# Optimization experiments

Hardware: AMD Instinct MI355X
Metric: run time of the kernel (lower is better)

The kernel has to match this reference:

```python
import jax, jax.numpy as jnp
import numpy as np

B, T, D, H = 4, 2048, 1024, 16
HD = D // H  # 64
EPS = 1e-5


def setup_inputs() -> dict:
    key = jax.random.key(0)
    ks = jax.random.split(key, 8)
    s = 0.02
    return {
        "X": jax.random.normal(ks[0], (B, T, D), dtype=jnp.float32),
        # per-head projection weights stacked: [H, D, HD] (no bias, matches nn.Linear(bias=False))
        "Wq": jax.random.normal(ks[1], (H, D, HD), dtype=jnp.float32) * s,
        "Wk": jax.random.normal(ks[2], (H, D, HD), dtype=jnp.float32) * s,
        "Wv": jax.random.normal(ks[3], (H, D, HD), dtype=jnp.float32) * s,
        "ln1_g": jnp.ones((D,), jnp.float32),
        "ln1_b": jnp.zeros((D,), jnp.float32),
        "W1": jax.random.normal(ks[4], (D, 4 * D), dtype=jnp.float32) * s,
        "b1": jnp.zeros((4 * D,), jnp.float32),
        "W2": jax.random.normal(ks[5], (4 * D, D), dtype=jnp.float32) * s,
        "b2": jnp.zeros((D,), jnp.float32),
        "ln2_g": jnp.ones((D,), jnp.float32),
        "ln2_b": jnp.zeros((D,), jnp.float32),
    }


def _layer_norm(x, g, b):
    m = jnp.mean(x, axis=-1, keepdims=True)
    v = jnp.mean((x - m) ** 2, axis=-1, keepdims=True)
    return (x - m) / jnp.sqrt(v + EPS) * g + b


def reference(X, Wq, Wk, Wv, ln1_g, ln1_b, W1, b1, W2, b2, ln2_g, ln2_b):
    # multi-head causal self-attention (naive full-matrix, matching source)
    Q = jnp.einsum('btd,hde->bhte', X, Wq)
    K = jnp.einsum('btd,hde->bhte', X, Wk)
    V = jnp.einsum('btd,hde->bhte', X, Wv)
    scores = jnp.einsum('bhte,bhse->bhts', Q, K) / jnp.sqrt(jnp.float32(HD))
    causal = jnp.tril(jnp.ones((T, T), dtype=bool))
    scores = jnp.where(causal, scores, jnp.finfo(scores.dtype).min)
    attn = jax.nn.softmax(scores, axis=-1)
    Yh = jnp.einsum('bhts,bhse->bhte', attn, V)  # [B,H,T,HD]
    Y = jnp.transpose(Yh, (0, 2, 1, 3)).reshape(B, T, D)  # concat heads

    X1 = _layer_norm(Y + X, ln1_g, ln1_b)
    ff = jax.nn.relu(X1 @ W1 + b1) @ W2 + b2  # dropout inactive (eval)
    X2 = ff + X1
    return _layer_norm(X2, ln2_g, ln2_b)
```

## Files before the change

kernel.cpp:

```cpp
#include <hip/hip_runtime.h>
#include <cstdint>


typedef _Float16 f16x8 __attribute__((ext_vector_type(8)));
typedef _Float16 f16x4 __attribute__((ext_vector_type(4)));
typedef float    f32x4 __attribute__((ext_vector_type(4)));

#define DEVI __device__ __forceinline__

typedef __attribute__((address_space(1))) uint32_t gas1_u32;
typedef __attribute__((address_space(3))) uint32_t las3_u32;

DEVI void gl2lds16(const void* g, void* l) {
  __builtin_amdgcn_global_load_lds((gas1_u32*)(uintptr_t)g,
                                   (las3_u32*)(uintptr_t)l, 16, 0, 0);
}

#define FENCE_BAR                                                            \
  __builtin_amdgcn_sched_barrier(0xF);                                       \
  __builtin_amdgcn_s_barrier();                                              \
  __builtin_amdgcn_sched_barrier(0xF);

__global__ __launch_bounds__(256) void preprocess(
    const float* __restrict__ X, _Float16* __restrict__ Xh,
    const float* __restrict__ Wq, const float* __restrict__ Wk,
    const float* __restrict__ Wv, _Float16* __restrict__ Wqkv,
    const float* __restrict__ W1, _Float16* __restrict__ W1t,
    const float* __restrict__ W2, _Float16* __restrict__ W2t) {
  const int idx = blockIdx.x;
  const int tid = threadIdx.x;
  if (idx < 4096) {
    const int i = (idx * 256 + tid) * 8;
    float4 a = *(const float4*)&X[i];
    float4 b = *(const float4*)&X[i + 4];
    f16x8 o;
    o[0] = (_Float16)a.x; o[1] = (_Float16)a.y; o[2] = (_Float16)a.z; o[3] = (_Float16)a.w;
    o[4] = (_Float16)b.x; o[5] = (_Float16)b.y; o[6] = (_Float16)b.z; o[7] = (_Float16)b.w;
    *(f16x8*)&Xh[i] = o;
    return;
  }
  __shared__ _Float16 T[64 * 72];
  const float* src;
  _Float16* dst;
  int k0, rowbase, stride, dstK;
  float scale = 1.0f;
  if (idx < 4864) {
    const int j = idx - 4096;
    const int z = j >> 4;
    const int which = z >> 4;
    const int slice = z & 15;
    src = ((which == 0) ? Wq : (which == 1) ? Wk : Wv) + (size_t)slice * 65536;
    scale = (which == 0) ? 0.18033688011112042f : 1.0f;
    k0 = (j & 15) * 64;
    rowbase = which * 1024 + slice * 64;
    stride = 64; dstK = 1024; dst = Wqkv;
  } else if (idx < 5888) {
    const int j = idx - 4864;
    src = W1 + (j >> 4) * 64;
    k0 = (j & 15) * 64;
    rowbase = (j >> 4) * 64;
    stride = 4096; dstK = 1024; dst = W1t;
  } else {
    const int j = idx - 5888;
    src = W2 + (j >> 6) * 64;
    k0 = (j & 63) * 64;
    rowbase = (j >> 6) * 64;
    stride = 1024; dstK = 4096; dst = W2t;
  }
#pragma unroll
  for (int p = 0; p < 4; ++p) {
    int c = p * 256 + tid;
    int kl = c >> 4;
    int nl = (c & 15) * 4;
    float4 v = *(const float4*)&src[(size_t)(k0 + kl) * stride + nl];
    T[(nl + 0) * 72 + kl] = (_Float16)(v.x * scale);
    T[(nl + 1) * 72 + kl] = (_Float16)(v.y * scale);
    T[(nl + 2) * 72 + kl] = (_Float16)(v.z * scale);
    T[(nl + 3) * 72 + kl] = (_Float16)(v.w * scale);
  }
  __syncthreads();
#pragma unroll
  for (int p = 0; p < 2; ++p) {
    int c = p * 256 + tid;
    int nl = c >> 3;
    int kc = (c & 7) * 8;
    f16x8 vv = *(const f16x8*)&T[nl * 72 + kc];
    *(f16x8*)&dst[(size_t)(rowbase + nl) * dstK + k0 + kc] = vv;
  }
}

__global__ __launch_bounds__(256) void transpose_v(
    const _Float16* __restrict__ Vh, _Float16* __restrict__ Vt) {
  __shared__ _Float16 T[64 * 72];
  const int t0 = blockIdx.x * 64;
  const size_t hb = (size_t)blockIdx.y * (2048 * 64);
  const int tid = threadIdx.x;
#pragma unroll
  for (int it = 0; it < 2; ++it) {
    const int c = it * 256 + tid;
    const int tl = c >> 3;
    const int ec = (c & 7) * 8;
    *(f16x8*)&T[tl * 72 + ec] =
        *(const f16x8*)&Vh[hb + (size_t)(t0 + tl) * 64 + ec];
  }
  __syncthreads();
#pragma unroll
  for (int it = 0; it < 2; ++it) {
    const int c = it * 256 + tid;
    const int el = c >> 3;
    const int tc = (c & 7) * 8;
    f16x8 o;
#pragma unroll
    for (int jj = 0; jj < 8; ++jj) o[jj] = T[(tc + jj) * 72 + el];
    *(f16x8*)&Vt[hb + (size_t)el * 2048 + t0 + tc] = o;
  }
}

template <int MODE>
__global__ __launch_bounds__(512, 1) void gemm8(
    const _Float16* __restrict__ A, const _Float16* __restrict__ Bt,
    int K, int N, int nbx, int cpx,
    const float* __restrict__ bias, _Float16* __restrict__ outH,
    _Float16* __restrict__ outQ, _Float16* __restrict__ outKp,
    _Float16* __restrict__ outV) {
  __shared__ _Float16 As[2][2][128 * 64];
  __shared__ _Float16 Bs[2][2][128 * 64];
  const int tid = threadIdx.x;
  const int lane = tid & 63;
  const int w = tid >> 6;
  const int wr = w >> 2, wc = w & 3;
  const int lr = lane & 15, g = lane >> 4;
  const int o = (blockIdx.x & 7) * cpx + (blockIdx.x >> 3);
  const int m0 = (o / nbx) * 256, n0 = (o % nbx) * 256;
  const int NT = K >> 6;

  const _Float16* Ab = A + (size_t)m0 * K;
  const _Float16* Bb = Bt + (size_t)n0 * K;

  f32x4 acc[8][4] = {};

  auto STG = [&](const _Float16* src, _Float16* dst) {
#pragma unroll
    for (int it = 0; it < 2; ++it) {
      const int c = it * 512 + tid;
      const int r = c >> 3;
      const int ts = (c & 7) ^ (r & 7);
      gl2lds16(src + (size_t)r * K + ts * 8, dst + c * 8);
    }
  };

  STG(Ab, &As[0][0][0]);
  STG(Ab + 128 * (size_t)K, &As[0][1][0]);
  STG(Bb, &Bs[0][0][0]);
  STG(Bb + 128 * (size_t)K, &Bs[0][1][0]);
  STG(Ab + 64, &As[1][0][0]);
  STG(Ab + 128 * (size_t)K + 64, &As[1][1][0]);
  STG(Bb + 64, &Bs[1][0][0]);
  asm volatile("s_waitcnt vmcnt(6)" ::: "memory");
  FENCE_BAR;

  f16x8 afA[4][2], afB[4][2], bfL[2][2], bfH[2][2];

#define LDA8_(af, MLO, buf)                                                  \
  _Pragma("unroll") for (int mf = 0; mf < 4; ++mf) {                         \
    const int rl = (MLO + mf) * 16 + lr;                                     \
    _Pragma("unroll") for (int k2 = 0; k2 < 2; ++k2)                         \
      af[mf][k2] = *(const f16x8*)&As[buf][wr][rl * 64 +                     \
                      (((k2 * 4 + g) ^ (rl & 7)) << 3)];                     \
  }
#define LDB8_(bf, NLO, buf)                                                  \
  _Pragma("unroll") for (int nf = 0; nf < 2; ++nf) {                         \
    const int rb = wc * 64 + (NLO + nf) * 16 + lr;                           \
    _Pragma("unroll") for (int k2 = 0; k2 < 2; ++k2)                         \
      bf[nf][k2] = *(const f16x8*)&Bs[buf][rb >> 7][(rb & 127) * 64 +        \
                      (((k2 * 4 + g) ^ (rb & 7)) << 3)];                     \
  }
#define MMA8_(af, bf, MB, NB)                                                \
  __builtin_amdgcn_s_setprio(1);                                             \
  _Pragma("unroll") for (int mf = 0; mf < 4; ++mf)                           \
  _Pragma("unroll") for (int nf = 0; nf < 2; ++nf)                           \
  _Pragma("unroll") for (int k2 = 0; k2 < 2; ++k2)                           \
    acc[(MB) + mf][(NB) + nf] = __builtin_amdgcn_mfma_f32_16x16x32_f16(      \
        af[mf][k2], bf[nf][k2], acc[(MB) + mf][(NB) + nf], 0, 0, 0);         \
  __builtin_amdgcn_s_setprio(0);

  for (int t = 0; t < NT; ++t) {
    const int cur = t & 1, nxt = cur ^ 1;
    LDA8_(afA, 0, cur);
    LDB8_(bfL, 0, cur);
    if (t + 1 < NT)
      STG(Bb + 128 * (size_t)K + (size_t)(t + 1) * 64, &Bs[nxt][1][0]);
    FENCE_BAR;
    MMA8_(afA, bfL, 0, 0);
    FENCE_BAR;
    LDA8_(afB, 4, cur);
    FENCE_BAR;
    MMA8_(afB, bfL, 4, 0);
    FENCE_BAR;
    LDB8_(bfH, 2, cur);
    if (t + 2 < NT) STG(Ab + (size_t)(t + 2) * 64, &As[cur][0][0]);
    FENCE_BAR;
    MMA8_(afA, bfH, 0, 2);
    FENCE_BAR;
    if (t + 2 < NT) {
      STG(Ab + 128 * (size_t)K + (size_t)(t + 2) * 64, &As[cur][1][0]);
      STG(Bb + (size_t)(t + 2) * 64, &Bs[cur][0][0]);
    }
    if (t == NT - 2) {
      asm volatile("s_waitcnt vmcnt(0)" ::: "memory");
    } else if (t < NT - 2) {
      asm volatile("s_waitcnt vmcnt(6)" ::: "memory");
    }
    FENCE_BAR;
    MMA8_(afB, bfH, 4, 2);
    FENCE_BAR;
  }
#undef LDA8_
#undef LDB8_
#undef MMA8_

#pragma unroll
  for (int mf = 0; mf < 8; ++mf) {
#pragma unroll
    for (int nf = 0; nf < 4; ++nf) {
#pragma unroll
      for (int rr = 0; rr < 4; ++rr) {
        const int row = m0 + wr * 128 + mf * 16 + g * 4 + rr;
        const int col = n0 + wc * 64 + nf * 16 + lr;
        const float v = acc[mf][nf][rr];
        if constexpr (MODE == 0) {
          const int qkv = col >> 10;
          const int h = (col >> 6) & 15;
          const int e = col & 63;
          const int bb = row >> 11;
          const int tt = row & 2047;
          const size_t idx = (((size_t)bb * 16 + h) * 2048 + tt) * 64 + e;
          const _Float16 hv = (_Float16)v;
          if (qkv == 0)      outQ[idx] = hv;
          else if (qkv == 1) outKp[idx] = hv;
          else               outV[idx] = hv;
        } else {
          outH[(size_t)row * N + col] =
              (_Float16)fmaxf(v + bias[col], 0.0f);
        }
      }
    }
  }
}

__global__ __launch_bounds__(512, 1) void gemm4_ffn2(
    const _Float16* __restrict__ A, const _Float16* __restrict__ Bt,
    int K, int N, int nbx, int cpx,
    const float* __restrict__ bias, const _Float16* __restrict__ residH,
    _Float16* __restrict__ outH) {
  __shared__ _Float16 As[2][2][128 * 64];
  __shared__ _Float16 Bs[2][128 * 64];
  const int tid = threadIdx.x;
  const int lane = tid & 63;
  const int w = tid >> 6;
  const int wr = w >> 1, wc = w & 1;
  const int lr = lane & 15, g = lane >> 4;
  const int o = (blockIdx.x & 7) * cpx + (blockIdx.x >> 3);
  const int m0 = (o / nbx) * 256, n0 = (o % nbx) * 128;
  const int NT = K >> 6;

  const _Float16* Ab = A + (size_t)m0 * K;
  const _Float16* Bb = Bt + (size_t)n0 * K;

  f32x4 acc[4][4] = {};

  auto STG = [&](const _Float16* src, _Float16* dst) {
#pragma unroll
    for (int it = 0; it < 2; ++it) {
      const int c = it * 512 + tid;
      const int r = c >> 3;
      const int ts = (c & 7) ^ (r & 7);
      gl2lds16(src + (size_t)r * K + ts * 8, dst + c * 8);
    }
  };

  STG(Ab, &As[0][0][0]);
  STG(Ab + 128 * (size_t)K, &As[0][1][0]);
  STG(Bb, &Bs[0][0]);
  STG(Ab + 64, &As[1][0][0]);
  STG(Ab + 128 * (size_t)K + 64, &As[1][1][0]);
  STG(Bb + 64, &Bs[1][0]);
  asm volatile("s_waitcnt vmcnt(6)" ::: "memory");
  FENCE_BAR;

  f16x8 af[4][2], bfL[2][2], bfH[2][2];

  for (int t = 0; t < NT; ++t) {
    const int b = t & 1;
#pragma unroll
    for (int mf = 0; mf < 4; ++mf) {
      const int rl = (wr & 1) * 64 + mf * 16 + lr;
#pragma unroll
      for (int k2 = 0; k2 < 2; ++k2)
        af[mf][k2] = *(const f16x8*)&As[b][wr >> 1]
            [rl * 64 + (((k2 * 4 + g) ^ (rl & 7)) << 3)];
    }
#pragma unroll
    for (int nf = 0; nf < 2; ++nf) {
      const int rb = wc * 64 + nf * 16 + lr;
#pragma unroll
      for (int k2 = 0; k2 < 2; ++k2)
        bfL[nf][k2] = *(const f16x8*)&Bs[b]
            [rb * 64 + (((k2 * 4 + g) ^ (rb & 7)) << 3)];
    }
    FENCE_BAR;
    if (t + 2 < NT) {
      STG(Ab + (size_t)(t + 2) * 64, &As[b][0][0]);
      STG(Ab + 128 * (size_t)K + (size_t)(t + 2) * 64, &As[b][1][0]);
    }
#pragma unroll
    for (int nf = 0; nf < 2; ++nf) {
      const int rb = wc * 64 + (nf + 2) * 16 + lr;
#pragma unroll
      for (int k2 = 0; k2 < 2; ++k2)
        bfH[nf][k2] = *(const f16x8*)&Bs[b]
            [rb * 64 + (((k2 * 4 + g) ^ (rb & 7)) << 3)];
    }
    __builtin_amdgcn_s_setprio(1);
#pragma unroll
    for (int mf = 0; mf < 4; ++mf)
#pragma unroll
      for (int nf = 0; nf < 2; ++nf)
#pragma unroll
        for (int k2 = 0; k2 < 2; ++k2)
          acc[mf][nf] = __builtin_amdgcn_mfma_f32_16x16x32_f16(
              af[mf][k2], bfL[nf][k2], acc[mf][nf], 0, 0, 0);
    __builtin_amdgcn_s_setprio(0);
    FENCE_BAR;
    if (t + 2 < NT) STG(Bb + (size_t)(t + 2) * 64, &Bs[b][0]);
    __builtin_amdgcn_s_setprio(1);
#pragma unroll
    for (int mf = 0; mf < 4; ++mf)
#pragma unroll
      for (int nf = 0; nf < 2; ++nf)
#pragma unroll
        for (int k2 = 0; k2 < 2; ++k2)
          acc[mf][nf + 2] = __builtin_amdgcn_mfma_f32_16x16x32_f16(
              af[mf][k2], bfH[nf][k2], acc[mf][nf + 2], 0, 0, 0);
    __builtin_amdgcn_s_setprio(0);
    if (t == NT - 2) {
      asm volatile("s_waitcnt vmcnt(0)" ::: "memory");
    } else if (t < NT - 2) {
      asm volatile("s_waitcnt vmcnt(6)" ::: "memory");
    }
    FENCE_BAR;
  }

#pragma unroll
  for (int mf = 0; mf < 4; ++mf) {
#pragma unroll
    for (int nf = 0; nf < 4; ++nf) {
#pragma unroll
      for (int rr = 0; rr < 4; ++rr) {
        const int row = m0 + wr * 64 + mf * 16 + g * 4 + rr;
        const int col = n0 + wc * 64 + nf * 16 + lr;
        outH[(size_t)row * N + col] = (_Float16)(
            acc[mf][nf][rr] + bias[col] +
            (float)residH[(size_t)row * N + col]);
      }
    }
  }
}

__global__ __launch_bounds__(256, 2) void attn_fwd9(
    const _Float16* __restrict__ Qg, const _Float16* __restrict__ Kg,
    const _Float16* __restrict__ Vtg, _Float16* __restrict__ Yg) {
  __shared__ _Float16 Ksm[2][64 * 64];
  __shared__ _Float16 Vts[2][64 * 64];
  __shared__ _Float16 Psm[128 * 72];
  const int tid = threadIdx.x;
  const int lane = tid & 63;
  const int w = tid >> 6;
  const int lr = lane & 15, g = lane >> 4;

  const int bid = blockIdx.x;
  const int bh  = (bid & 7) * 8 + ((bid >> 3) & 7);
  const int p   = bid >> 6;
  const int qtA = p, qtB = 15 - p;
  const int njA = 2 * p + 2;
  const int ntot = 34;

  const size_t hbo = (size_t)bh * (2048 * 64);
  const _Float16* Qb = Qg + hbo;
  const _Float16* Kb = Kg + hbo;
  const _Float16* Vb = Vtg + hbo;
  _Float16* Yb = Yg + hbo;

  f16x8 qfA[2][2], qfB[2][2];
#pragma unroll
  for (int mi = 0; mi < 2; ++mi) {
    const int rA = qtA * 128 + mi * 64 + w * 16 + lr;
    const int rB = qtB * 128 + mi * 64 + w * 16 + lr;
#pragma unroll
    for (int ss = 0; ss < 2; ++ss) {
      qfA[mi][ss] = *(const f16x8*)&Qb[(size_t)rA * 64 + ss * 32 + g * 8];
      qfB[mi][ss] = *(const f16x8*)&Qb[(size_t)rB * 64 + ss * 32 + g * 8];
    }
  }

  f32x4 accYA[2][4] = {}, accYB[2][4] = {};
  f32x4 accLA[2] = {}, accLB[2] = {};

  f16x8 ones;
#pragma unroll
  for (int i = 0; i < 8; ++i) ones[i] = (_Float16)1.0f;

  auto TK0 = [&](int u) { return (u < njA ? u : u - njA) * 64; };

  auto STAGE = [&](int bufi, int tk0) {
#pragma unroll
    for (int it = 0; it < 2; ++it) {
      const int c = it * 256 + tid;
      const int r = c >> 3;
      const int ts = (c & 7) ^ (r & 7);
      gl2lds16(Kb + (size_t)(tk0 + r) * 64 + ts * 8, &Ksm[bufi][c * 8]);
      gl2lds16(Vb + (size_t)r * 2048 + tk0 + ts * 8, &Vts[bufi][c * 8]);
    }
  };

  auto BODY = [&](int bufi, int qbase, int tk0, const f16x8 (&qf)[2][2],
                  f32x4 (&accY)[2][4], f32x4 (&accL)[2]) {
    const _Float16* Ks = Ksm[bufi];
    const _Float16* Vs = Vts[bufi];
    const int qlo0 = qbase + w * 16;
    const int qlo1 = qbase + 64 + w * 16;
    const bool act0 = (tk0 <= qlo0 + 15);
    f16x8 kf[4][2];
#pragma unroll
    for (int ni = 0; ni < 4; ++ni) {
      const int row = ni * 16 + lr;
#pragma unroll
      for (int kk = 0; kk < 2; ++kk)
        kf[ni][kk] = *(const f16x8*)&Ks[row * 64 + (((kk * 4 + g) ^ (row & 7)) << 3)];
    }
    f32x4 s0[4] = {}, s1[4] = {};
    __builtin_amdgcn_s_setprio(1);
    if (act0) {
#pragma unroll
      for (int ni = 0; ni < 4; ++ni)
#pragma unroll
        for (int kk = 0; kk < 2; ++kk)
          s0[ni] = __builtin_amdgcn_mfma_f32_16x16x32_f16(kf[ni][kk], qf[0][kk], s0[ni], 0, 0, 0);
    }
#pragma unroll
    for (int ni = 0; ni < 4; ++ni)
#pragma unroll
      for (int kk = 0; kk < 2; ++kk)
        s1[ni] = __builtin_amdgcn_mfma_f32_16x16x32_f16(kf[ni][kk], qf[1][kk], s1[ni], 0, 0, 0);
    __builtin_amdgcn_s_setprio(0);
    if (act0 && tk0 + 63 > qlo0) {
      const int qa = qlo0 + lr;
#pragma unroll
      for (int ni = 0; ni < 4; ++ni)
#pragma unroll
        for (int r = 0; r < 4; ++r)
          if (tk0 + ni * 16 + g * 4 + r > qa) s0[ni][r] = -3.0e38f;
    }
    if (tk0 + 63 > qlo1) {
      const int qa = qlo1 + lr;
#pragma unroll
      for (int ni = 0; ni < 4; ++ni)
#pragma unroll
        for (int r = 0; r < 4; ++r)
          if (tk0 + ni * 16 + g * 4 + r > qa) s1[ni][r] = -3.0e38f;
    }
    const int prow0 = w * 16 + lr;
    const int prow1 = 64 + w * 16 + lr;
    if (act0) {
#pragma unroll
      for (int ni = 0; ni < 4; ++ni) {
        auto a = __builtin_amdgcn_cvt_pkrtz(__builtin_amdgcn_exp2f(s0[ni][0]),
                                            __builtin_amdgcn_exp2f(s0[ni][1]));
        auto b = __builtin_amdgcn_cvt_pkrtz(__builtin_amdgcn_exp2f(s0[ni][2]),
                                            __builtin_amdgcn_exp2f(s0[ni][3]));
        f16x4 pk4;
        pk4[0] = a[0]; pk4[1] = a[1]; pk4[2] = b[0]; pk4[3] = b[1];
        *(f16x4*)&Psm[prow0 * 72 + ni * 16 + g * 4] = pk4;
      }
    }
#pragma unroll
    for (int ni = 0; ni < 4; ++ni) {
      auto a = __builtin_amdgcn_cvt_pkrtz(__builtin_amdgcn_exp2f(s1[ni][0]),
                                          __builtin_amdgcn_exp2f(s1[ni][1]));
      auto b = __builtin_amdgcn_cvt_pkrtz(__builtin_amdgcn_exp2f(s1[ni][2]),
                                          __builtin_amdgcn_exp2f(s1[ni][3]));
      f16x4 pk4;
      pk4[0] = a[0]; pk4[1] = a[1]; pk4[2] = b[0]; pk4[3] = b[1];
      *(f16x4*)&Psm[prow1 * 72 + ni * 16 + g * 4] = pk4;
    }
    __builtin_amdgcn_s_setprio(1);
#pragma unroll
    for (int ss = 0; ss < 2; ++ss) {
      f16x8 pa0 = {};
      f16x8 pa1 = *(const f16x8*)&Psm[prow1 * 72 + ss * 32 + g * 8];
      if (act0) pa0 = *(const f16x8*)&Psm[prow0 * 72 + ss * 32 + g * 8];
      if (act0) accL[0] = __builtin_amdgcn_mfma_f32_16x16x32_f16(pa0, ones, accL[0], 0, 0, 0);
      accL[1] = __builtin_amdgcn_mfma_f32_16x16x32_f16(pa1, ones, accL[1], 0, 0, 0);
#pragma unroll
      for (int ne = 0; ne < 4; ++ne) {
        const int vrow = ne * 16 + lr;
        const f16x8 vbf = *(const f16x8*)&Vs[vrow * 64 + (((ss * 4 + g) ^ (vrow & 7)) << 3)];
        if (act0) accY[0][ne] = __builtin_amdgcn_mfma_f32_16x16x32_f16(pa0, vbf, accY[0][ne], 0, 0, 0);
        accY[1][ne] = __builtin_amdgcn_mfma_f32_16x16x32_f16(pa1, vbf, accY[1][ne], 0, 0, 0);
      }
    }
    __builtin_amdgcn_s_setprio(0);
  };

  STAGE(0, TK0(0));
  for (int u = 0; u < ntot; ++u) {
    asm volatile("s_waitcnt vmcnt(0)" ::: "memory");
    __builtin_amdgcn_s_barrier();
    __builtin_amdgcn_sched_barrier(0xF);
    const int cur = u & 1;
    if (u + 1 < ntot) STAGE(cur ^ 1, TK0(u + 1));
    if (u < njA) BODY(cur, qtA * 128, u * 64, qfA, accYA, accLA);
    else         BODY(cur, qtB * 128, (u - njA) * 64, qfB, accYB, accLB);
  }

#pragma unroll
  for (int mi = 0; mi < 2; ++mi)
#pragma unroll
    for (int r = 0; r < 4; ++r) {
      const float invA = 1.0f / accLA[mi][r];
      const float invB = 1.0f / accLB[mi][r];
      const int qaA = qtA * 128 + mi * 64 + w * 16 + g * 4 + r;
      const int qaB = qtB * 128 + mi * 64 + w * 16 + g * 4 + r;
#pragma unroll
      for (int ne = 0; ne < 4; ++ne) {
        Yb[(size_t)qaA * 64 + ne * 16 + lr] = (_Float16)(accYA[mi][ne][r] * invA);
        Yb[(size_t)qaB * 64 + ne * 16 + lr] = (_Float16)(accYB[mi][ne][r] * invB);
      }
    }
}

__global__ __launch_bounds__(256) void ln1_fused(
    const _Float16* __restrict__ Yh, const _Float16* __restrict__ Xh,
    const float* __restrict__ gam, const float* __restrict__ bet,
    _Float16* __restrict__ X1h) {
  const int row = blockIdx.x;
  const int b = row >> 11, t = row & 2047;
  const int tid = threadIdx.x;
  const int d0 = tid * 4;
  const int h = d0 >> 6, e = d0 & 63;
  const f16x4 y4 = *(const f16x4*)&Yh[(((size_t)b * 16 + h) * 2048 + t) * 64 + e];
  const f16x4 x4 = *(const f16x4*)&Xh[(size_t)row * 1024 + d0];
  float v0 = (float)y4[0] + (float)x4[0], v1 = (float)y4[1] + (float)x4[1];
  float v2 = (float)y4[2] + (float)x4[2], v3 = (float)y4[3] + (float)x4[3];
  float s = v0 + v1 + v2 + v3;
  float q = v0 * v0 + v1 * v1 + v2 * v2 + v3 * v3;
  for (int off = 32; off; off >>= 1) { s += __shfl_xor(s, off); q += __shfl_xor(q, off); }
  __shared__ float red[8];
  const int w = tid >> 6;
  if ((tid & 63) == 0) { red[w] = s; red[4 + w] = q; }
  __syncthreads();
  s = red[0] + red[1] + red[2] + red[3];
  q = red[4] + red[5] + red[6] + red[7];
  const float mean = s * (1.f / 1024.f);
  const float rstd = rsqrtf(q * (1.f / 1024.f) - mean * mean + 1e-5f);
  const float4 G = *(const float4*)&gam[d0];
  const float4 Bv = *(const float4*)&bet[d0];
  f16x4 oh;
  oh[0] = (_Float16)((v0 - mean) * rstd * G.x + Bv.x);
  oh[1] = (_Float16)((v1 - mean) * rstd * G.y + Bv.y);
  oh[2] = (_Float16)((v2 - mean) * rstd * G.z + Bv.z);
  oh[3] = (_Float16)((v3 - mean) * rstd * G.w + Bv.w);
  *(f16x4*)&X1h[(size_t)row * 1024 + d0] = oh;
}

__global__ __launch_bounds__(256) void ln2_kernel(
    const _Float16* __restrict__ In, const float* __restrict__ gam,
    const float* __restrict__ bet, float* __restrict__ Out) {
  const int row = blockIdx.x;
  const int tid = threadIdx.x;
  const int d0 = tid * 4;
  const f16x4 v4 = *(const f16x4*)&In[(size_t)row * 1024 + d0];
  float v0 = (float)v4[0], v1 = (float)v4[1], v2 = (float)v4[2], v3 = (float)v4[3];
  float s = v0 + v1 + v2 + v3;
  float q = v0 * v0 + v1 * v1 + v2 * v2 + v3 * v3;
  for (int off = 32; off; off >>= 1) { s += __shfl_xor(s, off); q += __shfl_xor(q, off); }
  __shared__ float red[8];
  const int w = tid >> 6;
  if ((tid & 63) == 0) { red[w] = s; red[4 + w] = q; }
  __syncthreads();
  s = red[0] + red[1] + red[2] + red[3];
  q = red[4] + red[5] + red[6] + red[7];
  const float mean = s * (1.f / 1024.f);
  const float rstd = rsqrtf(q * (1.f / 1024.f) - mean * mean + 1e-5f);
  const float4 G = *(const float4*)&gam[d0];
  const float4 Bv = *(const float4*)&bet[d0];
  float4 o;
  o.x = (v0 - mean) * rstd * G.x + Bv.x;
  o.y = (v1 - mean) * rstd * G.y + Bv.y;
  o.z = (v2 - mean) * rstd * G.z + Bv.z;
  o.w = (v3 - mean) * rstd * G.w + Bv.w;
  *(float4*)&Out[(size_t)row * 1024 + d0] = o;
}

extern "C" void kernel_launch(void* const* d_in, const int* in_sizes, int n_in,
                              void* d_out, int out_size, void* d_ws, size_t ws_size,
                              hipStream_t stream) {
  (void)in_sizes; (void)n_in; (void)out_size; (void)ws_size;
  const float* X    = (const float*)d_in[0];
  const float* Wq   = (const float*)d_in[1];
  const float* Wk   = (const float*)d_in[2];
  const float* Wv   = (const float*)d_in[3];
  const float* ln1g = (const float*)d_in[4];
  const float* ln1b = (const float*)d_in[5];
  const float* W1   = (const float*)d_in[6];
  const float* b1   = (const float*)d_in[7];
  const float* W2   = (const float*)d_in[8];
  const float* b2   = (const float*)d_in[9];
  const float* ln2g = (const float*)d_in[10];
  const float* ln2b = (const float*)d_in[11];
  float* out = (float*)d_out;

  char* ws = (char*)d_ws;
  _Float16* Xh   = (_Float16*)(ws);
  _Float16* Qh   = (_Float16*)(ws + 16777216ull);
  _Float16* Kh   = (_Float16*)(ws + 33554432ull);
  _Float16* Vh   = (_Float16*)(ws + 50331648ull);
  _Float16* ff1  = (_Float16*)(ws);
  _Float16* Wqkv = (_Float16*)(ws + 67108864ull);
  _Float16* W1t  = (_Float16*)(ws + 73400320ull);
  _Float16* W2t  = (_Float16*)(ws + 81788928ull);
  _Float16* Yh   = (_Float16*)(ws + 90177536ull);
  _Float16* X2h  = (_Float16*)(ws + 90177536ull);
  _Float16* Vt   = (_Float16*)(ws + 106954752ull);
  _Float16* X1h  = (_Float16*)(ws + 157286400ull);

  preprocess<<<dim3(6912), dim3(256), 0, stream>>>(
      X, Xh, Wq, Wk, Wv, Wqkv, W1, W1t, W2, W2t);

  gemm8<0><<<dim3(384), dim3(512), 0, stream>>>(
      Xh, Wqkv, 1024, 3072, 12, 48, nullptr, nullptr, Qh, Kh, Vh);

  transpose_v<<<dim3(32, 64), dim3(256), 0, stream>>>(Vh, Vt);

  attn_fwd9<<<dim3(512), dim3(256), 0, stream>>>(Qh, Kh, Vt, Yh);

  ln1_fused<<<dim3(8192), dim3(256), 0, stream>>>(Yh, Xh, ln1g, ln1b, X1h);

  gemm8<1><<<dim3(512), dim3(512), 0, stream>>>(
      X1h, W1t, 1024, 4096, 16, 64, b1, ff1, nullptr, nullptr, nullptr);

  gemm4_ffn2<<<dim3(256), dim3(512), 0, stream>>>(
      ff1, W2t, 4096, 1024, 8, 32, b2, X1h, X2h);

  ln2_kernel<<<dim3(8192), dim3(256), 0, stream>>>(X2h, ln2g, ln2b, out);
}
```

Before: 318.8 us.

## Precompute LDS fragment pointers, unroll GEMM k-loop by two, reorder MFMA chains

In the big GEMM, LDS read addresses are precomputed once as per-lane byte pointers and the global-to-LDS staging offsets are hoisted out of the loop. The k-loop is unrolled by two so the double-buffer index becomes a compile-time constant. The combined fence-plus-barrier macros are replaced with plain barriers and explicit scheduling barriers around the staging loads. Across the GEMMs and attention, the MFMA loops are reordered so k2 is outermost, which interleaves independent accumulators instead of issuing back-to-back dependent MFMAs. The aim is less address arithmetic and fewer MFMA dependency stalls, at the cost of looser scheduling fences and the assumption that NT is even.

```diff
diff --git a/kernel.cpp b/kernel.cpp
--- a/kernel.cpp
+++ b/kernel.cpp
@@ -139,14 +139,27 @@
 
   f32x4 acc[8][4] = {};
 
-  auto STG = [&](const _Float16* src, _Float16* dst) {
-#pragma unroll
-    for (int it = 0; it < 2; ++it) {
-      const int c = it * 512 + tid;
-      const int r = c >> 3;
-      const int ts = (c & 7) ^ (r & 7);
-      gl2lds16(src + (size_t)r * K + ts * 8, dst + c * 8);
-    }
+  const int swz0 = ((g) ^ (lr & 7)) << 4;
+  const int swz1 = ((4 + g) ^ (lr & 7)) << 4;
+  const char* a0 = (const char*)(&As[0][0][0]) + wr * 16384 + lr * 128 + swz0;
+  const char* a1 = (const char*)(&As[0][0][0]) + wr * 16384 + lr * 128 + swz1;
+  const char* b0 = (const char*)(&Bs[0][0][0]) + wc * 8192 + lr * 128 + swz0;
+  const char* b1 = (const char*)(&Bs[0][0][0]) + wc * 8192 + lr * 128 + swz1;
+
+  int loff[2], doff[2];
+#pragma unroll
+  for (int it = 0; it < 2; ++it) {
+    const int c = it * 512 + tid;
+    const int r = c >> 3;
+    const int ts = (c & 7) ^ (r & 7);
+    loff[it] = r * K + ts * 8;
+    doff[it] = c * 8;
+  }
+
+  auto STG = [&](const _Float16* srcBase, _Float16* ldsBase) {
+#pragma unroll
+    for (int it = 0; it < 2; ++it)
+      gl2lds16(srcBase + loff[it], ldsBase + doff[it]);
   };
 
   STG(Ab, &As[0][0][0]);
@@ -161,63 +174,76 @@
 
   f16x8 afA[4][2], afB[4][2], bfL[2][2], bfH[2][2];
 
-#define LDA8_(af, MLO, buf)                                                  \
-  _Pragma("unroll") for (int mf = 0; mf < 4; ++mf) {                         \
-    const int rl = (MLO + mf) * 16 + lr;                                     \
-    _Pragma("unroll") for (int k2 = 0; k2 < 2; ++k2)                         \
-      af[mf][k2] = *(const f16x8*)&As[buf][wr][rl * 64 +                     \
-                      (((k2 * 4 + g) ^ (rl & 7)) << 3)];                     \
-  }
-#define LDB8_(bf, NLO, buf)                                                  \
-  _Pragma("unroll") for (int nf = 0; nf < 2; ++nf) {                         \
-    const int rb = wc * 64 + (NLO + nf) * 16 + lr;                           \
-    _Pragma("unroll") for (int k2 = 0; k2 < 2; ++k2)                         \
-      bf[nf][k2] = *(const f16x8*)&Bs[buf][rb >> 7][(rb & 127) * 64 +        \
-                      (((k2 * 4 + g) ^ (rb & 7)) << 3)];                     \
-  }
+#define LDA8P_(af, MLO, BUF)                                                 \
+  _Pragma("unroll") for (int k2 = 0; k2 < 2; ++k2)                           \
+  _Pragma("unroll") for (int mf = 0; mf < 4; ++mf)                           \
+    af[mf][k2] = *(const f16x8*)((k2 ? a1 : a0) +                            \
+                                 ((BUF)*32768 + ((MLO) + mf) * 2048));
+#define LDB8P_(bf, NLO, BUF)                                                 \
+  _Pragma("unroll") for (int k2 = 0; k2 < 2; ++k2)                           \
+  _Pragma("unroll") for (int nf = 0; nf < 2; ++nf)                           \
+    bf[nf][k2] = *(const f16x8*)((k2 ? b1 : b0) +                            \
+                                 ((BUF)*32768 + ((NLO) + nf) * 2048));
 #define MMA8_(af, bf, MB, NB)                                                \
   __builtin_amdgcn_s_setprio(1);                                             \
+  _Pragma("unroll") for (int k2 = 0; k2 < 2; ++k2)                           \
   _Pragma("unroll") for (int mf = 0; mf < 4; ++mf)                           \
   _Pragma("unroll") for (int nf = 0; nf < 2; ++nf)                           \
-  _Pragma("unroll") for (int k2 = 0; k2 < 2; ++k2)                           \
     acc[(MB) + mf][(NB) + nf] = __builtin_amdgcn_mfma_f32_16x16x32_f16(      \
         af[mf][k2], bf[nf][k2], acc[(MB) + mf][(NB) + nf], 0, 0, 0);         \
   __builtin_amdgcn_s_setprio(0);
-
-  for (int t = 0; t < NT; ++t) {
-    const int cur = t & 1, nxt = cur ^ 1;
-    LDA8_(afA, 0, cur);
-    LDB8_(bfL, 0, cur);
-    if (t + 1 < NT)
-      STG(Bb + 128 * (size_t)K + (size_t)(t + 1) * 64, &Bs[nxt][1][0]);
-    FENCE_BAR;
-    MMA8_(afA, bfL, 0, 0);
-    FENCE_BAR;
-    LDA8_(afB, 4, cur);
-    FENCE_BAR;
-    MMA8_(afB, bfL, 4, 0);
-    FENCE_BAR;
-    LDB8_(bfH, 2, cur);
-    if (t + 2 < NT) STG(Ab + (size_t)(t + 2) * 64, &As[cur][0][0]);
-    FENCE_BAR;
-    MMA8_(afA, bfH, 0, 2);
-    FENCE_BAR;
-    if (t + 2 < NT) {
-      STG(Ab + 128 * (size_t)K + (size_t)(t + 2) * 64, &As[cur][1][0]);
-      STG(Bb + (size_t)(t + 2) * 64, &Bs[cur][0][0]);
-    }
-    if (t == NT - 2) {
-      asm volatile("s_waitcnt vmcnt(0)" ::: "memory");
-    } else if (t < NT - 2) {
-      asm volatile("s_waitcnt vmcnt(6)" ::: "memory");
-    }
-    FENCE_BAR;
-    MMA8_(afB, bfH, 4, 2);
-    FENCE_BAR;
-  }
-#undef LDA8_
-#undef LDB8_
+#define BAR_ __builtin_amdgcn_s_barrier();
+#define SCHED0_ __builtin_amdgcn_sched_barrier(0);
+
+#define KTILE_(BUF, tt)                                                      \
+  {                                                                          \
+    LDA8P_(afA, 0, BUF);                                                     \
+    LDB8P_(bfL, 0, BUF);                                                     \
+    if ((tt) + 1 < NT) {                                                     \
+      SCHED0_;                                                               \
+      STG(Bb + 128 * (size_t)K + (size_t)((tt) + 1) * 64,                    \
+          &Bs[1 - (BUF)][1][0]);                                             \
+    }                                                                        \
+    BAR_;                                                                    \
+    MMA8_(afA, bfL, 0, 0);                                                   \
+    BAR_;                                                                    \
+    LDA8P_(afB, 4, BUF);                                                     \
+    BAR_;                                                                    \
+    MMA8_(afB, bfL, 4, 0);                                                   \
+    BAR_;                                                                    \
+    LDB8P_(bfH, 2, BUF);                                                     \
+    if ((tt) + 2 < NT) {                                                     \
+      SCHED0_;                                                               \
+      STG(Ab + (size_t)((tt) + 2) * 64, &As[BUF][0][0]);                     \
+    }                                                                        \
+    BAR_;                                                                    \
+    MMA8_(afA, bfH, 0, 2);                                                   \
+    BAR_;                                                                    \
+    if ((tt) + 2 < NT) {                                                     \
+      SCHED0_;                                                               \
+      STG(Ab + 128 * (size_t)K + (size_t)((tt) + 2) * 64, &As[BUF][1][0]);   \
+      STG(Bb + (size_t)((tt) + 2) * 64, &Bs[BUF][0][0]);                     \
+    }                                                                        \
+    if ((tt) == NT - 2) {                                                    \
+      asm volatile("s_waitcnt vmcnt(0)" ::: "memory");                       \
+    } else if ((tt) < NT - 2) {                                              \
+      asm volatile("s_waitcnt vmcnt(6)" ::: "memory");                       \
+    }                                                                        \
+    BAR_;                                                                    \
+    MMA8_(afB, bfH, 4, 2);                                                   \
+    BAR_;                                                                    \
+  }
+
+  for (int t = 0; t < NT; t += 2) {
+    KTILE_(0, t);
+    KTILE_(1, t + 1);
+  }
+#undef LDA8P_
+#undef LDB8P_
 #undef MMA8_
+#undef BAR_
+#undef SCHED0_
+#undef KTILE_
 
 #pragma unroll
   for (int mf = 0; mf < 8; ++mf) {
@@ -323,11 +349,11 @@
     }
     __builtin_amdgcn_s_setprio(1);
 #pragma unroll
-    for (int mf = 0; mf < 4; ++mf)
-#pragma unroll
-      for (int nf = 0; nf < 2; ++nf)
-#pragma unroll
-        for (int k2 = 0; k2 < 2; ++k2)
+    for (int k2 = 0; k2 < 2; ++k2)
+#pragma unroll
+      for (int mf = 0; mf < 4; ++mf)
+#pragma unroll
+        for (int nf = 0; nf < 2; ++nf)
           acc[mf][nf] = __builtin_amdgcn_mfma_f32_16x16x32_f16(
               af[mf][k2], bfL[nf][k2], acc[mf][nf], 0, 0, 0);
     __builtin_amdgcn_s_setprio(0);
@@ -335,11 +361,11 @@
     if (t + 2 < NT) STG(Bb + (size_t)(t + 2) * 64, &Bs[b][0]);
     __builtin_amdgcn_s_setprio(1);
 #pragma unroll
-    for (int mf = 0; mf < 4; ++mf)
-#pragma unroll
-      for (int nf = 0; nf < 2; ++nf)
-#pragma unroll
-        for (int k2 = 0; k2 < 2; ++k2)
+    for (int k2 = 0; k2 < 2; ++k2)
+#pragma unroll
+      for (int mf = 0; mf < 4; ++mf)
+#pragma unroll
+        for (int nf = 0; nf < 2; ++nf)
           acc[mf][nf + 2] = __builtin_amdgcn_mfma_f32_16x16x32_f16(
               af[mf][k2], bfH[nf][k2], acc[mf][nf + 2], 0, 0, 0);
     __builtin_amdgcn_s_setprio(0);
@@ -440,18 +466,17 @@
     }
     f32x4 s0[4] = {}, s1[4] = {};
     __builtin_amdgcn_s_setprio(1);
-    if (act0) {
+#pragma unroll
+    for (int kk = 0; kk < 2; ++kk) {
+      if (act0) {
+#pragma unroll
+        for (int ni = 0; ni < 4; ++ni)
+          s0[ni] = __builtin_amdgcn_mfma_f32_16x16x32_f16(kf[ni][kk], qf[0][kk], s0[ni], 0, 0, 0);
+      }
 #pragma unroll
       for (int ni = 0; ni < 4; ++ni)
-#pragma unroll
-        for (int kk = 0; kk < 2; ++kk)
-          s0[ni] = __builtin_amdgcn_mfma_f32_16x16x32_f16(kf[ni][kk], qf[0][kk], s0[ni], 0, 0, 0);
-    }
-#pragma unroll
-    for (int ni = 0; ni < 4; ++ni)
-#pragma unroll
-      for (int kk = 0; kk < 2; ++kk)
         s1[ni] = __builtin_amdgcn_mfma_f32_16x16x32_f16(kf[ni][kk], qf[1][kk], s1[ni], 0, 0, 0);
+    }
     __builtin_amdgcn_s_setprio(0);
     if (act0 && tk0 + 63 > qlo0) {
       const int qa = qlo0 + lr;
```

Result: no change. 318.3 us (-0.1%).
